# Performance work log

Measured on AMD Instinct MI355X. Metric: run time of the kernel, lower is better.

## Reference

```python
import jax, jax.numpy as jnp
import numpy as np

# ---- static config (matches init_kwargs) ----
N, E = 30000, 480000          # nodes, edges
H, T, ED = 128, 4, 16         # hidden, towers, edge_dim
F = H // T                    # per-tower channels = 32
NA, NS = 5, 3                 # num aggregators, num scalers

# prot_deg histogram: all nodes have degree 16 -> avg_deg['log'] = log(17)
_DEG_HIST = np.zeros(17, dtype=np.float64); _DEG_HIST[16] = N
AVG_DEG_LOG = float((np.log(np.arange(17) + 1.0) * _DEG_HIST).sum() / _DEG_HIST.sum())
LN_EPS = 1e-5
STD_EPS = 1e-5


def setup_inputs() -> dict:
    key = jax.random.key(0)
    ks = jax.random.split(key, 12)
    f32 = jnp.float32

    def lin_w(k, fi, fo, lead=()):
        return (jax.random.normal(k, lead + (fi, fo), f32) / np.sqrt(fi)).astype(f32)

    return {
        "x": jax.random.normal(ks[0], (N, H), f32),
        "prot_edge_index": jax.random.randint(ks[1], (2, E), 0, N, dtype=jnp.int32),
        "prot_edge_attr": jax.random.normal(ks[2], (E, ED), f32),
        # edge encoder Linear(ED -> F)
        "W_edge": lin_w(ks[3], ED, F), "b_edge": jnp.zeros((F,), f32),
        # per-tower pre MLP: Linear(3F -> F), ReLU, Linear(F -> F)
        "pre_W0": lin_w(ks[4], 3 * F, F, (T,)), "pre_b0": jnp.zeros((T, F), f32),
        "pre_W1": lin_w(ks[5], F, F, (T,)), "pre_b1": jnp.zeros((T, F), f32),
        # per-tower post MLP: Linear((NA*NS+1)*F -> F), ReLU, Linear(F -> F)
        "post_W0": lin_w(ks[6], (NA * NS + 1) * F, F, (T,)), "post_b0": jnp.zeros((T, F), f32),
        "post_W1": lin_w(ks[7], F, F, (T,)), "post_b1": jnp.zeros((T, F), f32),
        # final Linear(H -> H)
        "W_lin": lin_w(ks[8], H, H), "b_lin": jnp.zeros((H,), f32),
        # LayerNorm(H)
        "ln_g": jnp.ones((H,), f32), "ln_b": jnp.zeros((H,), f32),
    }


def _pna_block(x, src, dst, prot_edge_attr, W_edge, b_edge,
               pre_W0, pre_b0, pre_W1, pre_b1,
               post_W0, post_b0, post_W1, post_b1,
               W_lin, b_lin, ln_g, ln_b):
    xt = x.reshape(N, T, F)                                      # divide_input=True
    ea = prot_edge_attr @ W_edge + b_edge                        # [E, F]
    # message: cat([x_i, x_j, edge_attr]) per tower -> [E, T, 3F]
    h = jnp.concatenate(
        [xt[dst], xt[src], jnp.broadcast_to(ea[:, None, :], (E, T, F))], axis=-1)
    h = jax.nn.relu(jnp.einsum('etf,tfg->etg', h, pre_W0) + pre_b0)
    m = jnp.einsum('etf,tfg->etg', h, pre_W1) + pre_b1           # [E, T, F]

    # multi-aggregator scatter-reduce over destination nodes
    cnt = jax.ops.segment_sum(jnp.ones((E,), x.dtype), dst, num_segments=N)  # [N]
    denom = jnp.maximum(cnt, 1.0)[:, None, None]
    s = jax.ops.segment_sum(m, dst, num_segments=N)
    mean = s / denom
    has = (cnt > 0)[:, None, None]
    mn = jnp.where(has, jax.ops.segment_min(m, dst, num_segments=N), 0.0)
    mx = jnp.where(has, jax.ops.segment_max(m, dst, num_segments=N), 0.0)
    mean2 = jax.ops.segment_sum(m * m, dst, num_segments=N) / denom
    std = jnp.sqrt(jax.nn.relu(mean2 - mean * mean) + STD_EPS)
    agg = jnp.concatenate([s, mean, mn, mx, std], axis=-1)       # [N, T, 5F]

    # degree scalers: identity / amplification / attenuation
    deg = jnp.maximum(cnt, 1.0)[:, None, None]
    logd = jnp.log(deg + 1.0)
    out = jnp.concatenate(
        [agg, agg * (logd / AVG_DEG_LOG), agg * (AVG_DEG_LOG / logd)], axis=-1)  # [N,T,15F]

    # update: cat([x, out]) then per-tower post MLP
    out = jnp.concatenate([xt, out], axis=-1)                    # [N, T, 16F]
    out = jax.nn.relu(jnp.einsum('ntf,tfg->ntg', out, post_W0) + post_b0)
    out = jnp.einsum('ntf,tfg->ntg', out, post_W1) + post_b1     # [N, T, F]
    out = out.reshape(N, H) @ W_lin + b_lin                      # PNAConv output [N, H]

    # Protein_PNAConv wrapper: x + relu(LayerNorm(conv)); dropout is identity in eval
    mu = out.mean(-1, keepdims=True)
    var = jnp.mean((out - mu) ** 2, axis=-1, keepdims=True)
    ln = (out - mu) / jnp.sqrt(var + LN_EPS) * ln_g + ln_b
    return x + jax.nn.relu(ln)


def reference(x, prot_edge_index, prot_edge_attr, W_edge, b_edge,
              pre_W0, pre_b0, pre_W1, pre_b1,
              post_W0, post_b0, post_W1, post_b1,
              W_lin, b_lin, ln_g, ln_b):
    src, dst = prot_edge_index[0], prot_edge_index[1]
    return _pna_block(x, src, dst, prot_edge_attr, W_edge, b_edge,
                      pre_W0, pre_b0, pre_W1, pre_b1,
                      post_W0, post_b0, post_W1, post_b1,
                      W_lin, b_lin, ln_g, ln_b)
```

## Files before the change

kernel.cpp:

```cpp
#include <hip/hip_runtime.h>
#include <hip/hip_bf16.h>

#define NN 30000
#define NE 480000
#define ADL 2.8332133440562162f

typedef unsigned int u32;
typedef unsigned short u16;

typedef _Float16 half2v __attribute__((ext_vector_type(2)));

__device__ __forceinline__ u16 f2h(float f){
  union { _Float16 h; u16 u; } v; v.h = (_Float16)f; return v.u;
}
__device__ __forceinline__ float h2f_lo(u32 u){
  union { u16 us; _Float16 h; } v; v.us = (u16)(u & 0xffff); return (float)v.h;
}
__device__ __forceinline__ float h2f_hi(u32 u){
  union { u16 us; _Float16 h; } v; v.us = (u16)(u >> 16); return (float)v.h;
}
__device__ __forceinline__ u32 pack2(float lo, float hi){
  return (u32)f2h(lo) | ((u32)f2h(hi) << 16);
}
__device__ __forceinline__ float dot2f(u32 a, u32 b, float c){
#if defined(__has_builtin) && __has_builtin(__builtin_amdgcn_fdot2)
  union U { u32 u; half2v h; };
  U ua, ub; ua.u = a; ub.u = b;
  return __builtin_amdgcn_fdot2(ua.h, ub.h, c, false);
#else
  float r;
  asm("v_dot2_f32_f16 %0, %1, %2, %3" : "=v"(r) : "v"(a), "v"(b), "v"(c));
  return r;
#endif
}

__global__ void k_hist(const int* __restrict__ ei, int* __restrict__ cnt){
  int e = blockIdx.x * blockDim.x + threadIdx.x;
  if (e < NE) atomicAdd(&cnt[ei[NE + e]], 1);
}

__global__ __launch_bounds__(1024) void k_scanA(const int* __restrict__ cnt,
                                                int* __restrict__ off, int* __restrict__ bsum){
  __shared__ int buf[1024];
  const int b = blockIdx.x, tid = threadIdx.x;
  const int i = b*1024 + tid;
  int v = (i < NN) ? cnt[i] : 0;
  buf[tid] = v;
  __syncthreads();
  for (int s = 1; s < 1024; s <<= 1){
    int t = (tid >= s) ? buf[tid - s] : 0;
    __syncthreads();
    buf[tid] += t;
    __syncthreads();
  }
  if (i < NN) off[i] = buf[tid] - v;
  if (tid == 1023) bsum[b] = buf[1023];
}

__global__ void k_scanC(int* __restrict__ off, const int* __restrict__ bsum){
  int i = blockIdx.x * blockDim.x + threadIdx.x;
  if (i < NN){
    int pre = 0;
    const int nb = i >> 10;
    for (int b = 0; b < nb; ++b) pre += bsum[b];
    off[i] += pre;
  }
  if (i == NN) off[NN] = NE;
}

__global__ void k_scatter(const int* __restrict__ ei, const float* __restrict__ eattr,
                          const int* __restrict__ off,
                          int* __restrict__ cursor, int* __restrict__ eids,
                          int* __restrict__ sidC, u32* __restrict__ eattrH){
  int e = blockIdx.x * blockDim.x + threadIdx.x;
  if (e < NE){
    int d = ei[NE + e];
    int pos = off[d] + atomicAdd(&cursor[d], 1);
    eids[pos] = e;
    sidC[pos] = ei[e];
    const float* ar = eattr + (size_t)e * 16;
    u32* dst = eattrH + (size_t)pos * 8;
    #pragma unroll
    for (int q = 0; q < 8; ++q) dst[q] = pack2(ar[2*q], ar[2*q+1]);
  }
}

__global__ void k_prep(const float* __restrict__ x,
                       const float* __restrict__ preW0, const float* __restrict__ preW1,
                       const float* __restrict__ postW0, const float* __restrict__ postW1,
                       const float* __restrict__ Wlin,
                       const float* __restrict__ Wedge, const float* __restrict__ b_edge,
                       const float* __restrict__ pre_b0,
                       u32* __restrict__ preW0H, u32* __restrict__ preW1H,
                       u32* __restrict__ postW0H, u32* __restrict__ postW1H,
                       u32* __restrict__ WlinH,
                       u16* __restrict__ eaM16, float* __restrict__ pre_b0F,
                       u32* __restrict__ xH)
{
  int i = blockIdx.x * blockDim.x + threadIdx.x;
  if (i < NN * 64){
    const float2 v = *(const float2*)(x + (size_t)i * 2);
    xH[i] = pack2(v.x, v.y);
  }
  if (i < 32768){
    int c = i >> 8, q = i & 255;
    int t = c >> 5, f = c & 31;
    postW0H[i] = pack2(postW0[t*16384 + (2*q)*32 + f], postW0[t*16384 + (2*q+1)*32 + f]);
  }
  if (i < 8192){
    int c = i >> 6, q = i & 63;
    WlinH[i] = pack2(Wlin[(2*q)*128 + c], Wlin[(2*q+1)*128 + c]);
  }
  if (i < 4096){
    int c = i >> 5, q = i & 31;
    int t = c >> 5, f = c & 31;
    preW0H[i] = pack2(preW0[t*3072 + (2*q)*32 + f], preW0[t*3072 + (2*q+1)*32 + f]);
  }
  if (i < 2048){
    int c = i >> 4, q = i & 15;
    int t = c >> 5, f = c & 31;
    preW1H[i] = pack2(preW1[t*1024 + (2*q)*32 + f], preW1[t*1024 + (2*q+1)*32 + f]);
  }
  if (i < 2048){
    int c = i >> 4, q = i & 15;
    int t = c >> 5, f = c & 31;
    postW1H[i] = pack2(postW1[t*1024 + (2*q)*32 + f], postW1[t*1024 + (2*q+1)*32 + f]);
  }
  if (i < 2048){
    int c = i >> 4, kk = i & 15;
    int t = c >> 5, f = c & 31;
    float acc = 0.f;
    #pragma unroll 8
    for (int g = 0; g < 32; ++g)
      acc = fmaf(Wedge[kk*32 + g], preW0[t*3072 + (64+g)*32 + f], acc);
    eaM16[c*16 + kk] = f2h(acc);
  }
  if (i < 128){
    int t = i >> 5, f = i & 31;
    float acc = pre_b0[i];
    #pragma unroll 8
    for (int g = 0; g < 32; ++g)
      acc = fmaf(b_edge[g], preW0[t*3072 + (64+g)*32 + f], acc);
    pre_b0F[i] = acc;
  }
}

__global__ __launch_bounds__(128, 2) void k_edge4(
  const u32* __restrict__ xHu,
  const u32* __restrict__ atHu,
  const int* __restrict__ sidC,
  const u32* __restrict__ preW0H, const u32* __restrict__ preW1H,
  const u32* __restrict__ eaMu,
  const float* __restrict__ pre_b0F, const float* __restrict__ pre_b1,
  const int* __restrict__ off,
  u32* __restrict__ aggP)
{
  const int c = threadIdx.x;
  const int t = c >> 5;

  __shared__ __align__(16) u32 xdH[64];
  __shared__ __align__(16) u32 xsH[2][4][64];
  __shared__ __align__(16) u32 atS[2][4][8];
  __shared__ __align__(16) u32 hP[4][64];
  __shared__ int sidS[64];

  u32 w0p[32], w1p[16], wea[8];
  #pragma unroll
  for (int q = 0; q < 8; ++q) *(uint4*)&w0p[q*4] = *(const uint4*)(preW0H + (size_t)c*32 + q*4);
  #pragma unroll
  for (int q = 0; q < 4; ++q) *(uint4*)&w1p[q*4] = *(const uint4*)(preW1H + (size_t)c*16 + q*4);
  #pragma unroll
  for (int q = 0; q < 2; ++q) *(uint4*)&wea[q*4] = *(const uint4*)(eaMu + (size_t)c*8 + q*4);
  const float pb0 = pre_b0F[c];
  const float pb1 = pre_b1[c];

  const int el = c >> 6;
  const int eh = el + 2;
  const int col = c & 63;

  for (int nn = 0; nn < 8; ++nn){
    const int n = blockIdx.x * 8 + nn;
    __syncthreads();
    if (c < 64) xdH[c] = xHu[(size_t)n*64 + c];
    const int e0 = off[n], e1 = off[n+1];
    float sum = 0.f, sq = 0.f;
    float mn = __builtin_inff(), mx = -__builtin_inff();

    for (int base = e0; base < e1; base += 64){
      const int nv = min(64, e1 - base);
      if (c < nv) sidS[c] = sidC[base + c];
      __syncthreads();

      float a0n = pb0;
      #pragma unroll
      for (int i4 = 0; i4 < 4; ++i4){
        const uint4 xv = *(const uint4*)&xdH[t*16 + i4*4];
        a0n = dot2f(xv.x, w0p[i4*4+0], a0n);
        a0n = dot2f(xv.y, w0p[i4*4+1], a0n);
        a0n = dot2f(xv.z, w0p[i4*4+2], a0n);
        a0n = dot2f(xv.w, w0p[i4*4+3], a0n);
      }

      const int np = (nv + 3) >> 2;

      {
        const int g0 = min(el, nv-1), g1 = min(eh, nv-1);
        xsH[0][el][col] = xHu[(size_t)sidS[g0]*64 + col];
        xsH[0][eh][col] = xHu[(size_t)sidS[g1]*64 + col];
        if (c < 32){
          const int e = c >> 3, q = c & 7;
          atS[0][e][q] = atHu[(size_t)(base + min(e, nv-1))*8 + q];
        }
      }
      __syncthreads();

      for (int p = 0; p < np; ++p){
        const int buf = p & 1;
        const int sub = p * 4;
        const bool hasNext = (p + 1 < np);

        u32 nxs0 = 0, nxs1 = 0, nat = 0;
        if (hasNext){
          const int s2 = sub + 4;
          const int g0 = min(s2 + el, nv-1), g1 = min(s2 + eh, nv-1);
          nxs0 = xHu[(size_t)sidS[g0]*64 + col];
          nxs1 = xHu[(size_t)sidS[g1]*64 + col];
          if (c < 32){
            const int e = c >> 3, q = c & 7;
            nat = atHu[(size_t)(base + min(s2 + e, nv-1))*8 + q];
          }
        }

        float aXs[4] = {0,0,0,0}, aEa[4] = {0,0,0,0};
        #pragma unroll
        for (int i4 = 0; i4 < 4; ++i4){
          uint4 xsv[4];
          #pragma unroll
          for (int e = 0; e < 4; ++e)
            xsv[e] = *(const uint4*)&xsH[buf][e][t*16 + i4*4];
          const u32 wx0 = w0p[16+i4*4+0], wx1 = w0p[16+i4*4+1];
          const u32 wx2 = w0p[16+i4*4+2], wx3 = w0p[16+i4*4+3];
          #pragma unroll
          for (int e = 0; e < 4; ++e){
            aXs[e] = dot2f(xsv[e].x, wx0, aXs[e]);
            aXs[e] = dot2f(xsv[e].y, wx1, aXs[e]);
            aXs[e] = dot2f(xsv[e].z, wx2, aXs[e]);
            aXs[e] = dot2f(xsv[e].w, wx3, aXs[e]);
          }
        }
        #pragma unroll
        for (int i4 = 0; i4 < 2; ++i4){
          uint4 eav[4];
          #pragma unroll
          for (int e = 0; e < 4; ++e)
            eav[e] = *(const uint4*)&atS[buf][e][i4*4];
          const u32 we0 = wea[i4*4+0], we1 = wea[i4*4+1];
          const u32 we2 = wea[i4*4+2], we3 = wea[i4*4+3];
          #pragma unroll
          for (int e = 0; e < 4; ++e){
            aEa[e] = dot2f(eav[e].x, we0, aEa[e]);
            aEa[e] = dot2f(eav[e].y, we1, aEa[e]);
            aEa[e] = dot2f(eav[e].z, we2, aEa[e]);
            aEa[e] = dot2f(eav[e].w, we3, aEa[e]);
          }
        }
        #pragma unroll
        for (int e = 0; e < 4; ++e){
          const float h = fmaxf(a0n + aXs[e] + aEa[e], 0.f);
          const u32 mine = (u32)f2h(h);
          const u32 oth  = (u32)__shfl_xor((int)mine, 1);
          if ((c & 1) == 0) hP[e][c >> 1] = mine | (oth << 16);
        }

        float mm[4] = {pb1, pb1, pb1, pb1};
        #pragma unroll
        for (int i4 = 0; i4 < 4; ++i4){
          uint4 hv[4];
          #pragma unroll
          for (int e = 0; e < 4; ++e) hv[e] = *(const uint4*)&hP[e][t*16 + i4*4];
          const u32 w0v = w1p[i4*4+0], w1v = w1p[i4*4+1];
          const u32 w2v = w1p[i4*4+2], w3v = w1p[i4*4+3];
          #pragma unroll
          for (int e = 0; e < 4; ++e){
            mm[e] = dot2f(hv[e].x, w0v, mm[e]);
            mm[e] = dot2f(hv[e].y, w1v, mm[e]);
            mm[e] = dot2f(hv[e].z, w2v, mm[e]);
            mm[e] = dot2f(hv[e].w, w3v, mm[e]);
          }
        }
        #pragma unroll
        for (int e = 0; e < 4; ++e){
          if (sub + e < nv){
            sum += mm[e]; sq = fmaf(mm[e], mm[e], sq);
            mn = fminf(mn, mm[e]); mx = fmaxf(mx, mm[e]);
          }
        }

        if (hasNext){
          xsH[buf^1][el][col] = nxs0;
          xsH[buf^1][eh][col] = nxs1;
          if (c < 32){ const int e = c >> 3, q = c & 7; atS[buf^1][e][q] = nat; }
        }
        __syncthreads();
      }
    }

    const int deg = e1 - e0;
    const float mnz = (deg > 0) ? mn : 0.f;
    const float mxz = (deg > 0) ? mx : 0.f;
    const u32 sm = (u32)f2h(sum),  so = (u32)__shfl_xor((int)sm, 1);
    const u32 qm = (u32)f2h(sq),   qo = (u32)__shfl_xor((int)qm, 1);
    const u32 nm = (u32)f2h(mnz),  no = (u32)__shfl_xor((int)nm, 1);
    const u32 xm = (u32)f2h(mxz),  xo = (u32)__shfl_xor((int)xm, 1);
    if ((c & 1) == 0){
      const size_t b = (size_t)n * 256;
      const int j = c >> 1;
      aggP[b + j]        = sm | (so << 16);
      aggP[b + 64 + j]   = qm | (qo << 16);
      aggP[b + 128 + j]  = nm | (no << 16);
      aggP[b + 192 + j]  = xm | (xo << 16);
    }
  }
}

__global__ __launch_bounds__(128, 2) void k_post2(
  const float* __restrict__ x, const u32* __restrict__ xHu,
  const u32* __restrict__ aggP,
  const int* __restrict__ off,
  const u32* __restrict__ postW0H, const u32* __restrict__ postW1H,
  const u32* __restrict__ WlinH,
  const float* __restrict__ post_b0, const float* __restrict__ post_b1,
  const float* __restrict__ b_lin, const float* __restrict__ ln_g,
  const float* __restrict__ ln_b,
  float* __restrict__ out)
{
  const int c = threadIdx.x;
  const int t = c >> 5;
  const int n0 = blockIdx.x * 12;

  __shared__ __align__(16) u32 aS[12][384];
  __shared__ __align__(16) u32 hpP[12][64];
  __shared__ __align__(16) u32 vP[12][64];
  __shared__ __align__(16) float lnS[12][128];
  __shared__ float s1S[12], s2S[12], muS[12], rsS[12];

  {
    const int half = c >> 6, j = c & 63;
    #pragma unroll
    for (int k = 0; k < 6; ++k){
      const int n = half + k*2;
      const size_t nb = (size_t)(n0 + n);
      aS[n][j] = xHu[nb*64 + j];
      const u32 sp = aggP[nb*256 + j];
      const u32 qp = aggP[nb*256 + 64 + j];
      const int deg = off[n0+n+1] - off[n0+n];
      const float denom = fmaxf((float)deg, 1.f);
      const float s0 = h2f_lo(sp), s1v = h2f_hi(sp);
      const float q0 = h2f_lo(qp), q1v = h2f_hi(qp);
      const float me0 = s0 / denom, me1 = s1v / denom;
      const float sd0 = sqrtf(fmaxf(q0/denom - me0*me0, 0.f) + 1e-5f);
      const float sd1 = sqrtf(fmaxf(q1v/denom - me1*me1, 0.f) + 1e-5f);
      aS[n][64 + j]  = sp;
      aS[n][128 + j] = pack2(me0, me1);
      aS[n][192 + j] = aggP[nb*256 + 128 + j];
      aS[n][256 + j] = aggP[nb*256 + 192 + j];
      aS[n][320 + j] = pack2(sd0, sd1);
    }
  }
  if (c < 12){
    int deg = off[n0+c+1] - off[n0+c];
    float logd = logf(fmaxf((float)deg, 1.f) + 1.f);
    s1S[c] = logd / ADL; s2S[c] = ADL / logd;
  }
  __syncthreads();

  float acc[12], pa1[12], pa2[12];
  const float pb0 = post_b0[c];
  #pragma unroll
  for (int n = 0; n < 12; ++n){ acc[n] = pb0; pa1[n] = 0.f; pa2[n] = 0.f; }
  const u32* Wp = postW0H + (size_t)c * 256;
  #pragma unroll
  for (int q4 = 0; q4 < 4; ++q4){
    const uint4 w = *(const uint4*)(Wp + q4*4);
    #pragma unroll
    for (int n = 0; n < 12; ++n){
      const uint4 av = *(const uint4*)&aS[n][t*16 + q4*4];
      acc[n] = dot2f(av.x, w.x, acc[n]); acc[n] = dot2f(av.y, w.y, acc[n]);
      acc[n] = dot2f(av.z, w.z, acc[n]); acc[n] = dot2f(av.w, w.w, acc[n]);
    }
  }
  for (int a = 0; a < 5; ++a){
    #pragma unroll
    for (int q4 = 0; q4 < 4; ++q4){
      const uint4 wI = *(const uint4*)(Wp + 16  + a*16 + q4*4);
      const uint4 wA = *(const uint4*)(Wp + 96  + a*16 + q4*4);
      const uint4 wT = *(const uint4*)(Wp + 176 + a*16 + q4*4);
      #pragma unroll
      for (int n = 0; n < 12; ++n){
        const uint4 av = *(const uint4*)&aS[n][64 + a*64 + t*16 + q4*4];
        acc[n] = dot2f(av.x, wI.x, acc[n]); acc[n] = dot2f(av.y, wI.y, acc[n]);
        acc[n] = dot2f(av.z, wI.z, acc[n]); acc[n] = dot2f(av.w, wI.w, acc[n]);
        pa1[n] = dot2f(av.x, wA.x, pa1[n]); pa1[n] = dot2f(av.y, wA.y, pa1[n]);
        pa1[n] = dot2f(av.z, wA.z, pa1[n]); pa1[n] = dot2f(av.w, wA.w, pa1[n]);
        pa2[n] = dot2f(av.x, wT.x, pa2[n]); pa2[n] = dot2f(av.y, wT.y, pa2[n]);
        pa2[n] = dot2f(av.z, wT.z, pa2[n]); pa2[n] = dot2f(av.w, wT.w, pa2[n]);
      }
    }
  }
  #pragma unroll
  for (int n = 0; n < 12; ++n){
    const float hp = fmaxf(acc[n] + s1S[n]*pa1[n] + s2S[n]*pa2[n], 0.f);
    const u32 mine = (u32)f2h(hp);
    const u32 oth  = (u32)__shfl_xor((int)mine, 1);
    if ((c & 1) == 0) hpP[n][c >> 1] = mine | (oth << 16);
  }
  __syncthreads();

  u32 w1p2[16];
  #pragma unroll
  for (int q = 0; q < 4; ++q) *(uint4*)&w1p2[q*4] = *(const uint4*)(postW1H + (size_t)c*16 + q*4);
  const float pb1v = post_b1[c];
  #pragma unroll
  for (int n = 0; n < 12; ++n){
    float a2 = pb1v;
    #pragma unroll
    for (int q4 = 0; q4 < 4; ++q4){
      const uint4 hv = *(const uint4*)&hpP[n][t*16 + q4*4];
      a2 = dot2f(hv.x, w1p2[q4*4+0], a2); a2 = dot2f(hv.y, w1p2[q4*4+1], a2);
      a2 = dot2f(hv.z, w1p2[q4*4+2], a2); a2 = dot2f(hv.w, w1p2[q4*4+3], a2);
    }
    const u32 mine = (u32)f2h(a2);
    const u32 oth  = (u32)__shfl_xor((int)mine, 1);
    if ((c & 1) == 0) vP[n][c >> 1] = mine | (oth << 16);
  }
  __syncthreads();

  float a3[12];
  const float blv = b_lin[c];
  #pragma unroll
  for (int n = 0; n < 12; ++n) a3[n] = blv;
  const u32* Wl = WlinH + (size_t)c * 64;
  #pragma unroll 4
  for (int q4 = 0; q4 < 16; ++q4){
    const uint4 w = *(const uint4*)(Wl + q4*4);
    #pragma unroll
    for (int n = 0; n < 12; ++n){
      const uint4 vv = *(const uint4*)&vP[n][q4*4];
      a3[n] = dot2f(vv.x, w.x, a3[n]); a3[n] = dot2f(vv.y, w.y, a3[n]);
      a3[n] = dot2f(vv.z, w.z, a3[n]); a3[n] = dot2f(vv.w, w.w, a3[n]);
    }
  }

  #pragma unroll
  for (int n = 0; n < 12; ++n) lnS[n][c] = a3[n];
  __syncthreads();
  {
    const int n = c >> 3, seg = c & 7;
    if (n < 12){
      float ps = 0.f, ps2 = 0.f;
      #pragma unroll
      for (int k = 0; k < 16; ++k){
        float v = lnS[n][seg*16 + k];
        ps += v; ps2 = fmaf(v, v, ps2);
      }
      ps += __shfl_xor(ps, 1); ps2 += __shfl_xor(ps2, 1);
      ps += __shfl_xor(ps, 2); ps2 += __shfl_xor(ps2, 2);
      ps += __shfl_xor(ps, 4); ps2 += __shfl_xor(ps2, 4);
      if (seg == 0){
        float mu = ps * (1.f/128.f);
        float var = fmaxf(ps2 * (1.f/128.f) - mu*mu, 0.f);
        muS[n] = mu; rsS[n] = rsqrtf(var + 1e-5f);
      }
    }
  }
  __syncthreads();
  const float gv = ln_g[c], bv = ln_b[c];
  #pragma unroll
  for (int n = 0; n < 12; ++n){
    const size_t nb = (size_t)(n0 + n);
    float o = x[nb*128 + c] + fmaxf((a3[n] - muS[n])*rsS[n]*gv + bv, 0.f);
    out[nb*128 + c] = o;
  }
}

__global__ __launch_bounds__(128) void k_mono(
  const float* __restrict__ x, const int* __restrict__ ei,
  const float* __restrict__ eattr,
  const float* __restrict__ Wedge, const float* __restrict__ b_edge,
  const float* __restrict__ preW0, const float* __restrict__ pre_b0,
  const float* __restrict__ preW1, const float* __restrict__ pre_b1,
  const float* __restrict__ postW0, const float* __restrict__ post_b0,
  const float* __restrict__ postW1, const float* __restrict__ post_b1,
  const float* __restrict__ Wlin, const float* __restrict__ b_lin,
  const float* __restrict__ ln_g, const float* __restrict__ ln_b,
  const int* __restrict__ off, const int* __restrict__ eids,
  float* __restrict__ out)
{
  const int n = blockIdx.x;
  const int c = threadIdx.x;
  const int t = c >> 5, f = c & 31;
  __shared__ float xdS[128], xsS[128], eaS[32], hS[128];
  __shared__ float aggS[5][128], hpS[128], vS[128], red[4];

  const float xd = x[(size_t)n*128 + c];
  xdS[c] = xd;
  const int e0 = off[n], e1 = off[n+1];
  const int deg = e1 - e0;
  float sum = 0.f, sq = 0.f, mn = __builtin_inff(), mx = -__builtin_inff();
  __syncthreads();

  for (int idx = e0; idx < e1; ++idx){
    const int e = eids[idx];
    const int s = ei[e];
    xsS[c] = x[(size_t)s*128 + c];
    if (c < 32){
      float acc = b_edge[c];
      #pragma unroll
      for (int ii = 0; ii < 16; ++ii) acc = fmaf(eattr[(size_t)e*16 + ii], Wedge[ii*32 + c], acc);
      eaS[c] = acc;
    }
    __syncthreads();
    float acc = pre_b0[c];
    const float* W0 = preW0 + t*3072 + f;
    #pragma unroll 8
    for (int k = 0; k < 32; ++k) acc = fmaf(xdS[t*32+k], W0[k*32], acc);
    #pragma unroll 8
    for (int k = 0; k < 32; ++k) acc = fmaf(xsS[t*32+k], W0[(32+k)*32], acc);
    #pragma unroll 8
    for (int k = 0; k < 32; ++k) acc = fmaf(eaS[k], W0[(64+k)*32], acc);
    hS[c] = fmaxf(acc, 0.f);
    __syncthreads();
    float m = pre_b1[c];
    const float* W1 = preW1 + t*1024 + f;
    #pragma unroll 8
    for (int g = 0; g < 32; ++g) m = fmaf(hS[t*32+g], W1[g*32], m);
    sum += m; sq = fmaf(m, m, sq); mn = fminf(mn, m); mx = fmaxf(mx, m);
    __syncthreads();
  }
  const float d = (float)deg;
  const float denom = fmaxf(d, 1.f);
  const float mean = sum / denom;
  const float sd = sqrtf(fmaxf(sq/denom - mean*mean, 0.f) + 1e-5f);
  const float mnz = (deg > 0) ? mn : 0.f;
  const float mxz = (deg > 0) ? mx : 0.f;
  const float logd = logf(denom + 1.f);
  const float s1 = logd / ADL, s2 = ADL / logd;
  aggS[0][c] = sum; aggS[1][c] = mean; aggS[2][c] = mnz; aggS[3][c] = mxz; aggS[4][c] = sd;
  __syncthreads();
  float acc0 = post_b0[c];
  const float* P0 = postW0 + t*16384 + f;
  #pragma unroll 8
  for (int k = 0; k < 32; ++k) acc0 = fmaf(xdS[t*32+k], P0[k*32], acc0);
  float pa0 = 0.f, pa1 = 0.f, pa2 = 0.f;
  for (int a = 0; a < 5; ++a){
    const float* ag = &aggS[a][t*32];
    const float* Pb = P0 + (32 + a*32)*32;
    #pragma unroll 8
    for (int k = 0; k < 32; ++k){
      const float av = ag[k];
      pa0 = fmaf(av, Pb[k*32], pa0);
      pa1 = fmaf(av, Pb[(160+k)*32], pa1);
      pa2 = fmaf(av, Pb[(320+k)*32], pa2);
    }
  }
  hpS[c] = fmaxf(acc0 + pa0 + s1*pa1 + s2*pa2, 0.f);
  __syncthreads();
  float v = post_b1[c];
  const float* PW1 = postW1 + t*1024 + f;
  #pragma unroll 8
  for (int g = 0; g < 32; ++g) v = fmaf(hpS[t*32+g], PW1[g*32], v);
  vS[c] = v;
  __syncthreads();
  float l = b_lin[c];
  #pragma unroll 8
  for (int k = 0; k < 128; ++k) l = fmaf(vS[k], Wlin[k*128 + c], l);
  float ps = l, ps2 = l*l;
  #pragma unroll
  for (int o = 32; o >= 1; o >>= 1){ ps += __shfl_xor(ps, o); ps2 += __shfl_xor(ps2, o); }
  if ((c & 63) == 0){ red[c>>6] = ps; red[2 + (c>>6)] = ps2; }
  __syncthreads();
  const float mu = (red[0] + red[1]) * (1.f/128.f);
  const float var = fmaxf((red[2] + red[3]) * (1.f/128.f) - mu*mu, 0.f);
  const float rstd = rsqrtf(var + 1e-5f);
  out[(size_t)n*128 + c] = xd + fmaxf((l - mu)*rstd*ln_g[c] + ln_b[c], 0.f);
}

extern "C" void kernel_launch(void* const* d_in, const int* in_sizes, int n_in,
                              void* d_out, int out_size, void* d_ws, size_t ws_size,
                              hipStream_t stream){
  const float* x       = (const float*)d_in[0];
  const int*   ei      = (const int*)d_in[1];
  const float* eattr   = (const float*)d_in[2];
  const float* Wedge   = (const float*)d_in[3];
  const float* b_edge  = (const float*)d_in[4];
  const float* preW0   = (const float*)d_in[5];
  const float* pre_b0  = (const float*)d_in[6];
  const float* preW1   = (const float*)d_in[7];
  const float* pre_b1  = (const float*)d_in[8];
  const float* postW0  = (const float*)d_in[9];
  const float* post_b0 = (const float*)d_in[10];
  const float* postW1  = (const float*)d_in[11];
  const float* post_b1 = (const float*)d_in[12];
  const float* Wlin    = (const float*)d_in[13];
  const float* b_lin   = (const float*)d_in[14];
  const float* ln_g    = (const float*)d_in[15];
  const float* ln_b    = (const float*)d_in[16];

  char* ws = (char*)d_ws;
  size_t o = 0;
  auto alloc = [&](size_t bytes)->char*{
    char* p = ws + o; o = (o + bytes + 255) & ~((size_t)255); return p;
  };
  int* off    = (int*)alloc((NN + 1) * 4);
  int* cnt    = (int*)alloc(NN * 4);
  int* cursor = (int*)alloc(NN * 4);
  int* eids   = (int*)alloc(NE * 4);
  int* sidc   = (int*)alloc(NE * 4);
  int* bsum   = (int*)alloc(32 * 4);
  u32* preW0H  = (u32*)alloc(4096 * 4);
  u32* preW1H  = (u32*)alloc(2048 * 4);
  u32* postW0H = (u32*)alloc(32768 * 4);
  u32* postW1H = (u32*)alloc(2048 * 4);
  u32* WlinH   = (u32*)alloc(8192 * 4);
  u16* eaM16   = (u16*)alloc(2048 * 2);
  float* pre_b0F = (float*)alloc(128 * 4);
  u32* eattrH  = (u32*)alloc((size_t)NE * 8 * 4);
  u32* aggP    = (u32*)alloc((size_t)NN * 256 * 4);
  u32* xH      = (u32*)alloc((size_t)NN * 64 * 4);
  const size_t need = o;

  hipMemsetAsync(cnt, 0, NN * 4, stream);
  hipMemsetAsync(cursor, 0, NN * 4, stream);
  k_hist<<<(NE + 255)/256, 256, 0, stream>>>(ei, cnt);
  k_scanA<<<30, 1024, 0, stream>>>(cnt, off, bsum);
  k_scanC<<<(NN + 256)/256, 256, 0, stream>>>(off, bsum);
  k_scatter<<<(NE + 255)/256, 256, 0, stream>>>(ei, eattr, off, cursor, eids, sidc, eattrH);

  if (ws_size < need){
    k_mono<<<NN, 128, 0, stream>>>(x, ei, eattr, Wedge, b_edge,
                                   preW0, pre_b0, preW1, pre_b1,
                                   postW0, post_b0, postW1, post_b1,
                                   Wlin, b_lin, ln_g, ln_b,
                                   off, eids, (float*)d_out);
    return;
  }

  k_prep<<<(NN*64 + 255)/256, 256, 0, stream>>>(x, preW0, preW1, postW0, postW1, Wlin,
                                                Wedge, b_edge, pre_b0,
                                                preW0H, preW1H, postW0H, postW1H, WlinH,
                                                eaM16, pre_b0F, xH);
  k_edge4<<<NN/8, 128, 0, stream>>>(xH, eattrH, sidc, preW0H, preW1H,
                                    (const u32*)eaM16, pre_b0F, pre_b1, off, aggP);
  k_post2<<<NN/12, 128, 0, stream>>>(x, xH, aggP, off, postW0H, postW1H, WlinH,
                                     post_b0, post_b1, b_lin, ln_g, ln_b,
                                     (float*)d_out);
}
```

Before: 362.8 us.

## Fuse edge aggregation and post-MLP/LayerNorm into one per-block kernel

Merges the edge aggregation kernel and the post-processing kernel into one kernel that processes 8 nodes per block. Aggregates stay in shared memory instead of going through a global aggP buffer, and node features and offsets are preloaded into shared memory. This removes a global round-trip of 30000x256 words and one launch. The cost is more shared memory and registers per block, which may lower occupancy, and the post MLP now works on 8 nodes per block instead of 12.

```diff
diff --git a/kernel.cpp b/kernel.cpp
--- a/kernel.cpp
+++ b/kernel.cpp
@@ -145,24 +145,44 @@
   }
 }
 
-__global__ __launch_bounds__(128, 2) void k_edge4(
+__global__ __launch_bounds__(128, 2) void k_fused(
+  const float* __restrict__ x,
   const u32* __restrict__ xHu,
   const u32* __restrict__ atHu,
   const int* __restrict__ sidC,
   const u32* __restrict__ preW0H, const u32* __restrict__ preW1H,
   const u32* __restrict__ eaMu,
   const float* __restrict__ pre_b0F, const float* __restrict__ pre_b1,
+  const u32* __restrict__ postW0H, const u32* __restrict__ postW1H,
+  const u32* __restrict__ WlinH,
+  const float* __restrict__ post_b0, const float* __restrict__ post_b1,
+  const float* __restrict__ b_lin, const float* __restrict__ ln_g,
+  const float* __restrict__ ln_b,
   const int* __restrict__ off,
-  u32* __restrict__ aggP)
+  float* __restrict__ out)
 {
   const int c = threadIdx.x;
   const int t = c >> 5;
-
-  __shared__ __align__(16) u32 xdH[64];
+  const int n0 = blockIdx.x * 8;
+
+  __shared__ __align__(16) u32 xdA[8][64];
   __shared__ __align__(16) u32 xsH[2][4][64];
   __shared__ __align__(16) u32 atS[2][4][8];
   __shared__ __align__(16) u32 hP[4][64];
+  __shared__ __align__(16) u32 aggL[8][6][64];
+  __shared__ __align__(16) u32 hpP[8][64];
+  __shared__ __align__(16) u32 vP[8][64];
+  __shared__ __align__(16) float lnS[8][128];
   __shared__ int sidS[64];
+  __shared__ int offS[9];
+  __shared__ float s1S[8], s2S[8], muS[8], rsS[8];
+
+  #pragma unroll
+  for (int k = 0; k < 4; ++k){
+    const int idx = k*128 + c;
+    xdA[idx >> 6][idx & 63] = xHu[(size_t)(n0 + (idx >> 6))*64 + (idx & 63)];
+  }
+  if (c < 9) offS[c] = off[n0 + c];
 
   u32 w0p[32], w1p[16], wea[8];
   #pragma unroll
@@ -177,12 +197,11 @@
   const int el = c >> 6;
   const int eh = el + 2;
   const int col = c & 63;
+  __syncthreads();
 
   for (int nn = 0; nn < 8; ++nn){
-    const int n = blockIdx.x * 8 + nn;
     __syncthreads();
-    if (c < 64) xdH[c] = xHu[(size_t)n*64 + c];
-    const int e0 = off[n], e1 = off[n+1];
+    const int e0 = offS[nn], e1 = offS[nn+1];
     float sum = 0.f, sq = 0.f;
     float mn = __builtin_inff(), mx = -__builtin_inff();
 
@@ -194,7 +213,7 @@
       float a0n = pb0;
       #pragma unroll
       for (int i4 = 0; i4 < 4; ++i4){
-        const uint4 xv = *(const uint4*)&xdH[t*16 + i4*4];
+        const uint4 xv = *(const uint4*)&xdA[nn][t*16 + i4*4];
         a0n = dot2f(xv.x, w0p[i4*4+0], a0n);
         a0n = dot2f(xv.y, w0p[i4*4+1], a0n);
         a0n = dot2f(xv.z, w0p[i4*4+2], a0n);
@@ -313,78 +332,47 @@
     const u32 nm = (u32)f2h(mnz),  no = (u32)__shfl_xor((int)nm, 1);
     const u32 xm = (u32)f2h(mxz),  xo = (u32)__shfl_xor((int)xm, 1);
     if ((c & 1) == 0){
-      const size_t b = (size_t)n * 256;
       const int j = c >> 1;
-      aggP[b + j]        = sm | (so << 16);
-      aggP[b + 64 + j]   = qm | (qo << 16);
-      aggP[b + 128 + j]  = nm | (no << 16);
-      aggP[b + 192 + j]  = xm | (xo << 16);
-    }
-  }
-}
-
-__global__ __launch_bounds__(128, 2) void k_post2(
-  const float* __restrict__ x, const u32* __restrict__ xHu,
-  const u32* __restrict__ aggP,
-  const int* __restrict__ off,
-  const u32* __restrict__ postW0H, const u32* __restrict__ postW1H,
-  const u32* __restrict__ WlinH,
-  const float* __restrict__ post_b0, const float* __restrict__ post_b1,
-  const float* __restrict__ b_lin, const float* __restrict__ ln_g,
-  const float* __restrict__ ln_b,
-  float* __restrict__ out)
-{
-  const int c = threadIdx.x;
-  const int t = c >> 5;
-  const int n0 = blockIdx.x * 12;
-
-  __shared__ __align__(16) u32 aS[12][384];
-  __shared__ __align__(16) u32 hpP[12][64];
-  __shared__ __align__(16) u32 vP[12][64];
-  __shared__ __align__(16) float lnS[12][128];
-  __shared__ float s1S[12], s2S[12], muS[12], rsS[12];
-
-  {
-    const int half = c >> 6, j = c & 63;
-    #pragma unroll
-    for (int k = 0; k < 6; ++k){
-      const int n = half + k*2;
-      const size_t nb = (size_t)(n0 + n);
-      aS[n][j] = xHu[nb*64 + j];
-      const u32 sp = aggP[nb*256 + j];
-      const u32 qp = aggP[nb*256 + 64 + j];
-      const int deg = off[n0+n+1] - off[n0+n];
-      const float denom = fmaxf((float)deg, 1.f);
-      const float s0 = h2f_lo(sp), s1v = h2f_hi(sp);
-      const float q0 = h2f_lo(qp), q1v = h2f_hi(qp);
-      const float me0 = s0 / denom, me1 = s1v / denom;
-      const float sd0 = sqrtf(fmaxf(q0/denom - me0*me0, 0.f) + 1e-5f);
-      const float sd1 = sqrtf(fmaxf(q1v/denom - me1*me1, 0.f) + 1e-5f);
-      aS[n][64 + j]  = sp;
-      aS[n][128 + j] = pack2(me0, me1);
-      aS[n][192 + j] = aggP[nb*256 + 128 + j];
-      aS[n][256 + j] = aggP[nb*256 + 192 + j];
-      aS[n][320 + j] = pack2(sd0, sd1);
-    }
-  }
-  if (c < 12){
-    int deg = off[n0+c+1] - off[n0+c];
+      aggL[nn][0][j] = sm | (so << 16);
+      aggL[nn][5][j] = qm | (qo << 16);
+      aggL[nn][2][j] = nm | (no << 16);
+      aggL[nn][3][j] = xm | (xo << 16);
+    }
+  }
+
+  __syncthreads();
+  #pragma unroll
+  for (int k = 0; k < 4; ++k){
+    const int idx = k*128 + c;
+    const int n = idx >> 6, j = idx & 63;
+    const int deg = offS[n+1] - offS[n];
+    const float denom = fmaxf((float)deg, 1.f);
+    const u32 sp = aggL[n][0][j];
+    const u32 qp = aggL[n][5][j];
+    const float me0 = h2f_lo(sp)/denom, me1 = h2f_hi(sp)/denom;
+    const float sd0 = sqrtf(fmaxf(h2f_lo(qp)/denom - me0*me0, 0.f) + 1e-5f);
+    const float sd1 = sqrtf(fmaxf(h2f_hi(qp)/denom - me1*me1, 0.f) + 1e-5f);
+    aggL[n][1][j] = pack2(me0, me1);
+    aggL[n][4][j] = pack2(sd0, sd1);
+  }
+  if (c < 8){
+    int deg = offS[c+1] - offS[c];
     float logd = logf(fmaxf((float)deg, 1.f) + 1.f);
     s1S[c] = logd / ADL; s2S[c] = ADL / logd;
   }
   __syncthreads();
 
-  float acc[12], pa1[12], pa2[12];
-  const float pb0 = post_b0[c];
-  #pragma unroll
-  for (int n = 0; n < 12; ++n){ acc[n] = pb0; pa1[n] = 0.f; pa2[n] = 0.f; }
+  float acc[8], pa1[8], pa2[8];
+  const float pb0p = post_b0[c];
+  #pragma unroll
+  for (int n = 0; n < 8; ++n){ acc[n] = pb0p; pa1[n] = 0.f; pa2[n] = 0.f; }
   const u32* Wp = postW0H + (size_t)c * 256;
   #pragma unroll
   for (int q4 = 0; q4 < 4; ++q4){
     const uint4 w = *(const uint4*)(Wp + q4*4);
     #pragma unroll
-    for (int n = 0; n < 12; ++n){
-      const uint4 av = *(const uint4*)&aS[n][t*16 + q4*4];
+    for (int n = 0; n < 8; ++n){
+      const uint4 av = *(const uint4*)&xdA[n][t*16 + q4*4];
       acc[n] = dot2f(av.x, w.x, acc[n]); acc[n] = dot2f(av.y, w.y, acc[n]);
       acc[n] = dot2f(av.z, w.z, acc[n]); acc[n] = dot2f(av.w, w.w, acc[n]);
     }
@@ -396,8 +384,8 @@
       const uint4 wA = *(const uint4*)(Wp + 96  + a*16 + q4*4);
       const uint4 wT = *(const uint4*)(Wp + 176 + a*16 + q4*4);
       #pragma unroll
-      for (int n = 0; n < 12; ++n){
-        const uint4 av = *(const uint4*)&aS[n][64 + a*64 + t*16 + q4*4];
+      for (int n = 0; n < 8; ++n){
+        const uint4 av = *(const uint4*)&aggL[n][a][t*16 + q4*4];
         acc[n] = dot2f(av.x, wI.x, acc[n]); acc[n] = dot2f(av.y, wI.y, acc[n]);
         acc[n] = dot2f(av.z, wI.z, acc[n]); acc[n] = dot2f(av.w, wI.w, acc[n]);
         pa1[n] = dot2f(av.x, wA.x, pa1[n]); pa1[n] = dot2f(av.y, wA.y, pa1[n]);
@@ -408,7 +396,7 @@
     }
   }
   #pragma unroll
-  for (int n = 0; n < 12; ++n){
+  for (int n = 0; n < 8; ++n){
     const float hp = fmaxf(acc[n] + s1S[n]*pa1[n] + s2S[n]*pa2[n], 0.f);
     const u32 mine = (u32)f2h(hp);
     const u32 oth  = (u32)__shfl_xor((int)mine, 1);
@@ -416,18 +404,18 @@
   }
   __syncthreads();
 
-  u32 w1p2[16];
-  #pragma unroll
-  for (int q = 0; q < 4; ++q) *(uint4*)&w1p2[q*4] = *(const uint4*)(postW1H + (size_t)c*16 + q*4);
+  u32 w1q[16];
+  #pragma unroll
+  for (int q = 0; q < 4; ++q) *(uint4*)&w1q[q*4] = *(const uint4*)(postW1H + (size_t)c*16 + q*4);
   const float pb1v = post_b1[c];
   #pragma unroll
-  for (int n = 0; n < 12; ++n){
+  for (int n = 0; n < 8; ++n){
     float a2 = pb1v;
     #pragma unroll
     for (int q4 = 0; q4 < 4; ++q4){
       const uint4 hv = *(const uint4*)&hpP[n][t*16 + q4*4];
-      a2 = dot2f(hv.x, w1p2[q4*4+0], a2); a2 = dot2f(hv.y, w1p2[q4*4+1], a2);
-      a2 = dot2f(hv.z, w1p2[q4*4+2], a2); a2 = dot2f(hv.w, w1p2[q4*4+3], a2);
+      a2 = dot2f(hv.x, w1q[q4*4+0], a2); a2 = dot2f(hv.y, w1q[q4*4+1], a2);
+      a2 = dot2f(hv.z, w1q[q4*4+2], a2); a2 = dot2f(hv.w, w1q[q4*4+3], a2);
     }
     const u32 mine = (u32)f2h(a2);
     const u32 oth  = (u32)__shfl_xor((int)mine, 1);
@@ -435,16 +423,16 @@
   }
   __syncthreads();
 
-  float a3[12];
+  float a3[8];
   const float blv = b_lin[c];
   #pragma unroll
-  for (int n = 0; n < 12; ++n) a3[n] = blv;
+  for (int n = 0; n < 8; ++n) a3[n] = blv;
   const u32* Wl = WlinH + (size_t)c * 64;
   #pragma unroll 4
   for (int q4 = 0; q4 < 16; ++q4){
     const uint4 w = *(const uint4*)(Wl + q4*4);
     #pragma unroll
-    for (int n = 0; n < 12; ++n){
+    for (int n = 0; n < 8; ++n){
       const uint4 vv = *(const uint4*)&vP[n][q4*4];
       a3[n] = dot2f(vv.x, w.x, a3[n]); a3[n] = dot2f(vv.y, w.y, a3[n]);
       a3[n] = dot2f(vv.z, w.z, a3[n]); a3[n] = dot2f(vv.w, w.w, a3[n]);
@@ -452,34 +440,32 @@
   }
 
   #pragma unroll
-  for (int n = 0; n < 12; ++n) lnS[n][c] = a3[n];
+  for (int n = 0; n < 8; ++n) lnS[n][c] = a3[n];
   __syncthreads();
   {
-    const int n = c >> 3, seg = c & 7;
-    if (n < 12){
-      float ps = 0.f, ps2 = 0.f;
-      #pragma unroll
-      for (int k = 0; k < 16; ++k){
-        float v = lnS[n][seg*16 + k];
-        ps += v; ps2 = fmaf(v, v, ps2);
-      }
-      ps += __shfl_xor(ps, 1); ps2 += __shfl_xor(ps2, 1);
-      ps += __shfl_xor(ps, 2); ps2 += __shfl_xor(ps2, 2);
-      ps += __shfl_xor(ps, 4); ps2 += __shfl_xor(ps2, 4);
-      if (seg == 0){
-        float mu = ps * (1.f/128.f);
-        float var = fmaxf(ps2 * (1.f/128.f) - mu*mu, 0.f);
-        muS[n] = mu; rsS[n] = rsqrtf(var + 1e-5f);
-      }
+    const int n = c >> 4, seg = c & 15;
+    float ps = 0.f, ps2 = 0.f;
+    #pragma unroll
+    for (int k = 0; k < 8; ++k){
+      float v = lnS[n][seg*8 + k];
+      ps += v; ps2 = fmaf(v, v, ps2);
+    }
+    ps += __shfl_xor(ps, 1); ps2 += __shfl_xor(ps2, 1);
+    ps += __shfl_xor(ps, 2); ps2 += __shfl_xor(ps2, 2);
+    ps += __shfl_xor(ps, 4); ps2 += __shfl_xor(ps2, 4);
+    ps += __shfl_xor(ps, 8); ps2 += __shfl_xor(ps2, 8);
+    if (seg == 0){
+      float mu = ps * (1.f/128.f);
+      float var = fmaxf(ps2 * (1.f/128.f) - mu*mu, 0.f);
+      muS[n] = mu; rsS[n] = rsqrtf(var + 1e-5f);
     }
   }
   __syncthreads();
   const float gv = ln_g[c], bv = ln_b[c];
   #pragma unroll
-  for (int n = 0; n < 12; ++n){
+  for (int n = 0; n < 8; ++n){
     const size_t nb = (size_t)(n0 + n);
-    float o = x[nb*128 + c] + fmaxf((a3[n] - muS[n])*rsS[n]*gv + bv, 0.f);
-    out[nb*128 + c] = o;
+    out[nb*128 + c] = x[nb*128 + c] + fmaxf((a3[n] - muS[n])*rsS[n]*gv + bv, 0.f);
   }
 }
 
@@ -625,7 +611,6 @@
   u16* eaM16   = (u16*)alloc(2048 * 2);
   float* pre_b0F = (float*)alloc(128 * 4);
   u32* eattrH  = (u32*)alloc((size_t)NE * 8 * 4);
-  u32* aggP    = (u32*)alloc((size_t)NN * 256 * 4);
   u32* xH      = (u32*)alloc((size_t)NN * 64 * 4);
   const size_t need = o;
 
@@ -649,9 +634,9 @@
                                                 Wedge, b_edge, pre_b0,
                                                 preW0H, preW1H, postW0H, postW1H, WlinH,
                                                 eaM16, pre_b0F, xH);
-  k_edge4<<<NN/8, 128, 0, stream>>>(xH, eattrH, sidc, preW0H, preW1H,
-                                    (const u32*)eaM16, pre_b0F, pre_b1, off, aggP);
-  k_post2<<<NN/12, 128, 0, stream>>>(x, xH, aggP, off, postW0H, postW1H, WlinH,
-                                     post_b0, post_b1, b_lin, ln_g, ln_b,
-                                     (float*)d_out);
-}
+  k_fused<<<NN/8, 128, 0, stream>>>(x, xH, eattrH, sidc, preW0H, preW1H,
+                                    (const u32*)eaM16, pre_b0F, pre_b1,
+                                    postW0H, postW1H, WlinH,
+                                    post_b0, post_b1, b_lin, ln_g, ln_b,
+                                    off, (float*)d_out);
+}
```

Result: slower. 372.0 us (+2.5%).
